# Performance work log

Hardware: AMD Instinct MI355X
Metric: run time of the kernel (lower is better)

## Reference

```python
import jax, jax.numpy as jnp
import numpy as np

N_NODES = 100000
N_EDGES = 3200000
FEAT = 16


def gcn_conv(x, src, dst, W, b):
    # PyG GCNConv: add self-loops, symmetric normalization deg^{-1/2}(A+I)deg^{-1/2},
    # then linear transform and scatter-add aggregation.
    n = x.shape[0]
    loop = jnp.arange(n, dtype=src.dtype)
    s = jnp.concatenate([src, loop])
    d = jnp.concatenate([dst, loop])
    deg = jax.ops.segment_sum(jnp.ones_like(d, dtype=x.dtype), d, num_segments=n)
    dinv = jnp.where(deg > 0, jax.lax.rsqrt(deg), 0.0)
    norm = dinv[s] * dinv[d]  # [E+N]
    h = x @ W  # [N, out]
    msg = h[s] * norm[:, None]  # gather + weight
    out = jax.ops.segment_sum(msg, d, num_segments=n)  # scatter-add
    return out + b


def setup_inputs() -> dict:
    key = jax.random.key(0)
    k1, k2, k3, k4 = jax.random.split(key, 4)
    scale = 1.0 / np.sqrt(FEAT)
    return {
        "x": jax.random.normal(k1, (N_NODES, FEAT), dtype=jnp.float32),
        "edge_index": jax.random.randint(k2, (2, N_EDGES), 0, N_NODES, dtype=jnp.int64) if jax.config.jax_enable_x64 else jax.random.randint(k2, (2, N_EDGES), 0, N_NODES, dtype=jnp.int32),
        "W1": jax.random.normal(k3, (FEAT, 16), dtype=jnp.float32) * scale,
        "b1": jnp.zeros((16,), dtype=jnp.float32),
        "W2": jax.random.normal(k4, (16, FEAT), dtype=jnp.float32) * scale,
        "b2": jnp.zeros((FEAT,), dtype=jnp.float32),
    }


def reference(x, edge_index, W1, b1, W2, b2):
    src, dst = edge_index[0], edge_index[1]
    h = gcn_conv(x, src, dst, W1, b1)
    h = jax.nn.relu(h)
    out = gcn_conv(h, src, dst, W2, b2)
    return out
```

## Files before the change

### kernel.cpp

```cpp
#include <hip/hip_runtime.h>

#define F 16
#define BSHIFT 8
#define NPB 256
#define NB 391
#define CH 4096
#define BCAP 9216


__global__ void init_cursor_kernel(unsigned* __restrict__ cursor) {
    int i = threadIdx.x;
    if (i < NB) cursor[i * 16] = (unsigned)(i * BCAP);
}

__global__ __launch_bounds__(512) void
reorder_kernel(const int* __restrict__ src, const int* __restrict__ dst,
               unsigned* __restrict__ cursor, unsigned* __restrict__ recs, int E) {
    __shared__ unsigned lsorted[CH];
    __shared__ unsigned short lbkt[CH];
    __shared__ unsigned cnt[NB];
    __shared__ unsigned lstart[NB + 1];
    int t = threadIdx.x, b = blockIdx.x;
    int e0 = b * CH;
    int cnt_e = E - e0; if (cnt_e > CH) cnt_e = CH;

    for (int i = t; i < NB; i += 512) cnt[i] = 0;
    __syncthreads();
    unsigned pk[8], rs[8];
#pragma unroll
    for (int j = 0; j < 8; ++j) {
        int i = t + j * 512;
        pk[j] = 0xFFFFFFFFu;
        if (i < cnt_e) {
            unsigned d = (unsigned)dst[e0 + i];
            rs[j] = (unsigned)src[e0 + i];
            unsigned bk = d >> BSHIFT;
            unsigned r = atomicAdd(&cnt[bk], 1u);
            pk[j] = bk | ((d & 255u) << 9) | (r << 17);
        }
    }
    __syncthreads();
    if (t < 64) {
        unsigned run = 0;
        for (int c = 0; c < NB; c += 64) {
            int idx = c + t;
            unsigned v = (idx < NB) ? cnt[idx] : 0u;
            unsigned inc = v;
#pragma unroll
            for (int d = 1; d < 64; d <<= 1) {
                unsigned o = __shfl_up(inc, d, 64);
                if (t >= d) inc += o;
            }
            if (idx < NB) lstart[idx] = run + inc - v;
            run += __shfl(inc, 63, 64);
        }
        if (t == 0) lstart[NB] = (unsigned)cnt_e;
    }
    __syncthreads();
    {
        int s0 = (int)(((unsigned)b * 101u) % (unsigned)NB);
        for (int q = t; q < NB; q += 512) {
            int i = s0 + q; if (i >= NB) i -= NB;
            unsigned c = cnt[i];
            if (c) cnt[i] = atomicAdd(&cursor[i * 16], c);
        }
    }
    __syncthreads();
#pragma unroll
    for (int j = 0; j < 8; ++j) {
        int i = t + j * 512;
        if (i < cnt_e) {
            unsigned p = pk[j];
            unsigned bk = p & 0x1FFu;
            unsigned pos = lstart[bk] + (p >> 17);
            lsorted[pos] = rs[j] | (((p >> 9) & 255u) << 17);
            lbkt[pos] = (unsigned short)bk;
        }
    }
    __syncthreads();
    for (int i = t; i < cnt_e; i += 512) {
        unsigned bk = lbkt[i];
        recs[cnt[bk] + ((unsigned)i - lstart[bk])] = lsorted[i];
    }
}

__global__ __launch_bounds__(1024) void
sort2_kernel(const unsigned* __restrict__ recs, const unsigned* __restrict__ cursor,
             unsigned* __restrict__ srcs, int* __restrict__ noff, int* __restrict__ nend,
             float* __restrict__ dinv, const float* __restrict__ x,
             float* __restrict__ z, int n) {
    __shared__ unsigned lsort[BCAP];
    __shared__ unsigned cnt[NPB];
    __shared__ unsigned ex[NPB];
    __shared__ float ldv[NPB];
    __shared__ unsigned wtot[4];
    int t = threadIdx.x, b = blockIdx.x;
    int e0 = b * BCAP;
    int used = (int)(cursor[b * 16] - (unsigned)e0);
    if (t < NPB) cnt[t] = 0;
    __syncthreads();
    unsigned pk[9], rsr[9];
#pragma unroll
    for (int j = 0; j < 9; ++j) {
        int i = t + j * 1024;
        pk[j] = 0xFFFFFFFFu;
        if (i < used) {
            unsigned rec = recs[e0 + i];
            unsigned node = rec >> 17;
            rsr[j] = rec;
            unsigned r = atomicAdd(&cnt[node], 1u);
            pk[j] = node | (r << 8);
        }
    }
    __syncthreads();
    if (t < NPB) {
        unsigned c = cnt[t];
        unsigned inc = c;
        int lane = t & 63, w = t >> 6;
#pragma unroll
        for (int d = 1; d < 64; d <<= 1) {
            unsigned o = __shfl_up(inc, d, 64);
            if (lane >= d) inc += o;
        }
        if (lane == 63) wtot[w] = inc;
        __syncthreads();
        unsigned wbase = 0;
        for (int i = 0; i < w; ++i) wbase += wtot[i];
        unsigned e = wbase + inc - c;
        ex[t] = e;
        float dv = rsqrtf((float)c + 1.0f);
        ldv[t] = dv;
        int node = b * NPB + t;
        if (node < n) {
            noff[node] = e0 + (int)e;
            nend[node] = e0 + (int)(e + c);
            dinv[node] = dv;
        }
    } else {
        __syncthreads();
    }
    __syncthreads();
#pragma unroll
    for (int j = 0; j < 9; ++j) {
        int i = t + j * 1024;
        if (i < used) {
            unsigned p = pk[j];
            lsort[ex[p & 255u] + (p >> 8)] = rsr[j];
        }
    }
    __syncthreads();
    for (int i = t; i < used; i += 1024) srcs[e0 + i] = lsort[i];
    {
        int node = b * NPB + (t >> 2);
        if (node < n) {
            float4 v = ((const float4*)x)[(size_t)b * 1024 + t];
            float dv = ldv[t >> 2];
            v.x *= dv; v.y *= dv; v.z *= dv; v.w *= dv;
            ((float4*)z)[(size_t)b * 1024 + t] = v;
        }
    }
}

__global__ __launch_bounds__(256) void
agg_bal_kernel(const float* __restrict__ hin, const unsigned* __restrict__ srcs,
               const int* __restrict__ noff, const int* __restrict__ nend,
               const float* __restrict__ dinv,
               const float* __restrict__ W, const float* __restrict__ bias,
               float* __restrict__ outp, int n, int mode) {
    __shared__ float acc[64][F + 1];
    __shared__ float Ws[F * F];
    int t = threadIdx.x, b = blockIdx.x;
    int g = t >> 2, c = t & 3;
    Ws[t] = W[t];
    for (int i = t; i < 64 * (F + 1); i += 256) ((float*)acc)[i] = 0.f;
    __syncthreads();
    int nfirst = b * 64;
    int nlast = nfirst + 63; if (nlast > n - 1) nlast = n - 1;
    int e_start = noff[nfirst];
    int e_end = nend[nlast];
    int T = e_end - e_start;
    int chunk = (T + 63) >> 6;
    int gs = e_start + g * chunk;
    int ge = gs + chunk; if (ge > e_end) ge = e_end;
    const float4* h4 = (const float4*)hin;

#define PROC(r, v)                                                        \
    {                                                                     \
        int nd = (int)((r >> 17) & 63u);                                  \
        if (nd != cur) {                                                  \
            float* a = &acc[cur][c * 4];                                  \
            atomicAdd(a + 0, s.x); atomicAdd(a + 1, s.y);                 \
            atomicAdd(a + 2, s.z); atomicAdd(a + 3, s.w);                 \
            s.x = 0.f; s.y = 0.f; s.z = 0.f; s.w = 0.f;                   \
            cur = nd;                                                     \
        }                                                                 \
        s.x += v.x; s.y += v.y; s.z += v.z; s.w += v.w;                   \
    }

    if (gs < ge) {
        int cur = (int)((srcs[gs] >> 17) & 63u);
        float4 s = {0.f, 0.f, 0.f, 0.f};
        int e = gs;
        for (; e + 4 <= ge; e += 4) {
            unsigned r0 = srcs[e], r1 = srcs[e + 1], r2 = srcs[e + 2], r3 = srcs[e + 3];
            float4 v0 = h4[(size_t)(r0 & 0x1FFFFu) * 4 + c];
            float4 v1 = h4[(size_t)(r1 & 0x1FFFFu) * 4 + c];
            float4 v2 = h4[(size_t)(r2 & 0x1FFFFu) * 4 + c];
            float4 v3 = h4[(size_t)(r3 & 0x1FFFFu) * 4 + c];
            PROC(r0, v0); PROC(r1, v1); PROC(r2, v2); PROC(r3, v3);
        }
        for (; e < ge; ++e) {
            unsigned r0 = srcs[e];
            float4 v0 = h4[(size_t)(r0 & 0x1FFFFu) * 4 + c];
            PROC(r0, v0);
        }
        float* a = &acc[cur][c * 4];
        atomicAdd(a + 0, s.x); atomicAdd(a + 1, s.y);
        atomicAdd(a + 2, s.z); atomicAdd(a + 3, s.w);
    }
#undef PROC
    __syncthreads();
    int node = nfirst + g;
    if (node < n) {
        float4 self = h4[(size_t)node * 4 + c];
        float* ar = &acc[g][c * 4];
        ar[0] += self.x; ar[1] += self.y; ar[2] += self.z; ar[3] += self.w;
    }
    __syncthreads();
    if (node < n) {
        float di = dinv[node];
        float4 o = {0.f, 0.f, 0.f, 0.f};
        int j = c * 4;
#pragma unroll
        for (int k = 0; k < F; ++k) {
            float ak = acc[g][k];
            o.x += ak * Ws[k * F + j + 0];
            o.y += ak * Ws[k * F + j + 1];
            o.z += ak * Ws[k * F + j + 2];
            o.w += ak * Ws[k * F + j + 3];
        }
        float4 bi = ((const float4*)bias)[c];
        o.x = di * o.x + bi.x; o.y = di * o.y + bi.y;
        o.z = di * o.z + bi.z; o.w = di * o.w + bi.w;
        if (mode == 1) {
            o.x = fmaxf(o.x, 0.f) * di; o.y = fmaxf(o.y, 0.f) * di;
            o.z = fmaxf(o.z, 0.f) * di; o.w = fmaxf(o.w, 0.f) * di;
        }
        ((float4*)outp)[(size_t)node * 4 + c] = o;
    }
}


__global__ void deg_kernel(const int* __restrict__ dst, float* __restrict__ deg, int E) {
    int e = blockIdx.x * blockDim.x + threadIdx.x;
    if (e < E) atomicAdd(&deg[dst[e]], 1.0f);
}
__global__ void dinv_kernel(float* __restrict__ deg, int n) {
    int i = blockIdx.x * blockDim.x + threadIdx.x;
    if (i < n) deg[i] = rsqrtf(deg[i] + 1.0f);
}
__global__ void linear2_kernel(const float* __restrict__ in, const float* __restrict__ acc,
                               const float* __restrict__ dinv, const float* __restrict__ W,
                               const float* __restrict__ bias, float* __restrict__ out,
                               int n, int mode) {
    __shared__ float Ws[F * F];
    __shared__ float As[16][F + 1];
    int t = threadIdx.x;
    Ws[t] = W[t];
    int nb = t >> 4, j = t & 15;
    int i = blockIdx.x * 16 + nb;
    float di = 0.f, v = 0.f;
    if (i < n) {
        di = dinv[i]; v = in[i * F + j];
        if (mode) { v = di * (acc[i * F + j] + v) + bias[j]; v = fmaxf(v, 0.f); }
    }
    As[nb][j] = v;
    __syncthreads();
    if (i < n) {
        float s = 0.f;
#pragma unroll
        for (int k = 0; k < F; ++k) s += As[nb][k] * Ws[k * F + j];
        out[i * F + j] = s * di;
    }
}
__global__ void scatter_kernel(const int* __restrict__ src, const int* __restrict__ dst,
                               const float* __restrict__ h, float* __restrict__ acc, int E) {
    int t = blockIdx.x * blockDim.x + threadIdx.x;
    int e = t >> 4, j = t & 15;
    if (e < E) atomicAdd(&acc[dst[e] * F + j], h[src[e] * F + j]);
}
__global__ void out_kernel(const float* __restrict__ acc, const float* __restrict__ h,
                           const float* __restrict__ dinv, const float* __restrict__ bias,
                           float* __restrict__ out, int n) {
    int t = blockIdx.x * blockDim.x + threadIdx.x;
    if (t < n * F) {
        int i = t >> 4, j = t & 15;
        out[t] = dinv[i] * (acc[t] + h[t]) + bias[j];
    }
}


extern "C" void kernel_launch(void* const* d_in, const int* in_sizes, int n_in,
                              void* d_out, int out_size, void* d_ws, size_t ws_size,
                              hipStream_t stream) {
    const float* x  = (const float*)d_in[0];
    const int*   ei = (const int*)d_in[1];
    const float* W1 = (const float*)d_in[2];
    const float* b1 = (const float*)d_in[3];
    const float* W2 = (const float*)d_in[4];
    const float* b2 = (const float*)d_in[5];
    float* outp = (float*)d_out;

    const int N = in_sizes[0] / F;
    const int E = in_sizes[1] / 2;
    const int* src = ei;
    const int* dst = ei + E;

    const int nb_rt = (N + NPB - 1) >> BSHIFT;
    const size_t RC = (size_t)NB * BCAP;
    size_t need = sizeof(unsigned) * ((size_t)N * 19 + 2 * RC + 16 * NB);

    if (nb_rt == NB && E <= CH * 65535 && ws_size >= need) {
        float* dinv = (float*)d_ws;
        float* z = dinv + N;
        unsigned* recs = (unsigned*)(z + (size_t)F * N);
        float* y = (float*)recs;
        unsigned* srcs = recs + RC;
        int* noff = (int*)(srcs + RC);
        int* nend = noff + N;
        unsigned* cursor = (unsigned*)(nend + N);

        init_cursor_kernel<<<1, 512, 0, stream>>>(cursor);
        reorder_kernel<<<(E + CH - 1) / CH, 512, 0, stream>>>(src, dst, cursor, recs, E);
        sort2_kernel<<<NB, 1024, 0, stream>>>(recs, cursor, srcs, noff, nend, dinv, x, z, N);
        agg_bal_kernel<<<(N + 63) / 64, 256, 0, stream>>>(z, srcs, noff, nend, dinv, W1, b1, y, N, 1);
        agg_bal_kernel<<<(N + 63) / 64, 256, 0, stream>>>(y, srcs, noff, nend, dinv, W2, b2, outp, N, 2);
    } else {
        float* dinv = (float*)d_ws;
        float* h = dinv + N;
        float* acc = h + (size_t)F * N;
        hipMemsetAsync(dinv, 0, (size_t)N * sizeof(float), stream);
        hipMemsetAsync(acc, 0, (size_t)F * N * sizeof(float), stream);
        deg_kernel<<<(E + 255) / 256, 256, 0, stream>>>(dst, dinv, E);
        dinv_kernel<<<(N + 255) / 256, 256, 0, stream>>>(dinv, N);
        linear2_kernel<<<(N + 15) / 16, 256, 0, stream>>>(x, nullptr, dinv, W1, nullptr, h, N, 0);
        scatter_kernel<<<((size_t)E * F + 255) / 256, 256, 0, stream>>>(src, dst, h, acc, E);
        linear2_kernel<<<(N + 15) / 16, 256, 0, stream>>>(h, acc, dinv, W2, b1, h, N, 1);
        hipMemsetAsync(acc, 0, (size_t)F * N * sizeof(float), stream);
        scatter_kernel<<<((size_t)E * F + 255) / 256, 256, 0, stream>>>(src, dst, h, acc, E);
        out_kernel<<<((size_t)N * F + 255) / 256, 256, 0, stream>>>(acc, h, dinv, b2, outp, N);
    }
}
```

Baseline: 210.1 us.

## Fuse per-node sort into aggregation kernel, splitting each bucket into four quarter-blocks

```diff
diff --git a/kernel.cpp b/kernel.cpp
--- a/kernel.cpp
+++ b/kernel.cpp
@@ -6,6 +6,7 @@
 #define NB 391
 #define CH 4096
 #define BCAP 9216
+#define QCAP 2432
 
 
 __global__ void init_cursor_kernel(unsigned* __restrict__ cursor) {
@@ -85,104 +86,94 @@
 }
 
 __global__ __launch_bounds__(1024) void
-sort2_kernel(const unsigned* __restrict__ recs, const unsigned* __restrict__ cursor,
-             unsigned* __restrict__ srcs, int* __restrict__ noff, int* __restrict__ nend,
-             float* __restrict__ dinv, const float* __restrict__ x,
-             float* __restrict__ z, int n) {
-    __shared__ unsigned lsort[BCAP];
+histz_kernel(const unsigned* __restrict__ recs, const unsigned* __restrict__ cursor,
+             const float* __restrict__ x, float* __restrict__ z, int n) {
     __shared__ unsigned cnt[NPB];
-    __shared__ unsigned ex[NPB];
     __shared__ float ldv[NPB];
-    __shared__ unsigned wtot[4];
     int t = threadIdx.x, b = blockIdx.x;
     int e0 = b * BCAP;
     int used = (int)(cursor[b * 16] - (unsigned)e0);
     if (t < NPB) cnt[t] = 0;
     __syncthreads();
-    unsigned pk[9], rsr[9];
-#pragma unroll
-    for (int j = 0; j < 9; ++j) {
-        int i = t + j * 1024;
-        pk[j] = 0xFFFFFFFFu;
-        if (i < used) {
-            unsigned rec = recs[e0 + i];
-            unsigned node = rec >> 17;
-            rsr[j] = rec;
-            unsigned r = atomicAdd(&cnt[node], 1u);
-            pk[j] = node | (r << 8);
-        }
-    }
-    __syncthreads();
-    if (t < NPB) {
-        unsigned c = cnt[t];
-        unsigned inc = c;
-        int lane = t & 63, w = t >> 6;
+    for (int i = t; i < used; i += 1024)
+        atomicAdd(&cnt[recs[e0 + i] >> 17], 1u);
+    __syncthreads();
+    if (t < NPB) ldv[t] = rsqrtf((float)cnt[t] + 1.0f);
+    __syncthreads();
+    int node = b * NPB + (t >> 2);
+    if (node < n) {
+        float4 v = ((const float4*)x)[(size_t)b * 1024 + t];
+        float dv = ldv[t >> 2];
+        v.x *= dv; v.y *= dv; v.z *= dv; v.w *= dv;
+        ((float4*)z)[(size_t)b * 1024 + t] = v;
+    }
+}
+
+__global__ __launch_bounds__(256) void
+agg_fused_kernel(const float* __restrict__ hin, const unsigned* __restrict__ recs,
+                 const unsigned* __restrict__ cursor,
+                 const float* __restrict__ W, const float* __restrict__ bias,
+                 float* __restrict__ outp, int n, int mode) {
+    __shared__ unsigned lraw[QCAP];
+    __shared__ unsigned lsort[QCAP];
+    __shared__ float acc[64][F + 1];
+    __shared__ float Ws[F * F];
+    __shared__ unsigned cnt[64];
+    __shared__ unsigned ex[64];
+    __shared__ float ldv[64];
+    __shared__ unsigned nloc_s;
+    int t = threadIdx.x, b = blockIdx.x;
+    int bucket = b >> 2, q = b & 3;
+    int e0 = bucket * BCAP;
+    int used = (int)(cursor[bucket * 16] - (unsigned)e0);
+    int lane = t & 63;
+    Ws[t] = W[t];
+    if (t < 64) cnt[t] = 0;
+    if (t == 0) nloc_s = 0;
+    for (int i = t; i < 64 * (F + 1); i += 256) ((float*)acc)[i] = 0.f;
+    __syncthreads();
+    for (int i = t; i < used; i += 256) {
+        unsigned rec = recs[e0 + i];
+        unsigned node = rec >> 17;
+        bool mine = ((node >> 6) == (unsigned)q);
+        unsigned long long m = __ballot(mine);
+        if (m) {
+            int ldr = __ffsll((long long)m) - 1;
+            unsigned base = 0;
+            if (lane == ldr) base = atomicAdd(&nloc_s, (unsigned)__popcll(m));
+            base = __shfl(base, ldr, 64);
+            if (mine) {
+                unsigned pre = (unsigned)__popcll(m & ((1ull << lane) - 1ull));
+                lraw[base + pre] = rec;
+                atomicAdd(&cnt[node & 63u], 1u);
+            }
+        }
+    }
+    __syncthreads();
+    int nloc = (int)nloc_s;
+    if (t < 64) {
+        unsigned c0 = cnt[t];
+        unsigned inc = c0;
 #pragma unroll
         for (int d = 1; d < 64; d <<= 1) {
             unsigned o = __shfl_up(inc, d, 64);
-            if (lane >= d) inc += o;
-        }
-        if (lane == 63) wtot[w] = inc;
-        __syncthreads();
-        unsigned wbase = 0;
-        for (int i = 0; i < w; ++i) wbase += wtot[i];
-        unsigned e = wbase + inc - c;
-        ex[t] = e;
-        float dv = rsqrtf((float)c + 1.0f);
-        ldv[t] = dv;
-        int node = b * NPB + t;
-        if (node < n) {
-            noff[node] = e0 + (int)e;
-            nend[node] = e0 + (int)(e + c);
-            dinv[node] = dv;
-        }
-    } else {
-        __syncthreads();
-    }
-    __syncthreads();
-#pragma unroll
-    for (int j = 0; j < 9; ++j) {
-        int i = t + j * 1024;
-        if (i < used) {
-            unsigned p = pk[j];
-            lsort[ex[p & 255u] + (p >> 8)] = rsr[j];
-        }
-    }
-    __syncthreads();
-    for (int i = t; i < used; i += 1024) srcs[e0 + i] = lsort[i];
-    {
-        int node = b * NPB + (t >> 2);
-        if (node < n) {
-            float4 v = ((const float4*)x)[(size_t)b * 1024 + t];
-            float dv = ldv[t >> 2];
-            v.x *= dv; v.y *= dv; v.z *= dv; v.w *= dv;
-            ((float4*)z)[(size_t)b * 1024 + t] = v;
-        }
-    }
-}
-
-__global__ __launch_bounds__(256) void
-agg_bal_kernel(const float* __restrict__ hin, const unsigned* __restrict__ srcs,
-               const int* __restrict__ noff, const int* __restrict__ nend,
-               const float* __restrict__ dinv,
-               const float* __restrict__ W, const float* __restrict__ bias,
-               float* __restrict__ outp, int n, int mode) {
-    __shared__ float acc[64][F + 1];
-    __shared__ float Ws[F * F];
-    int t = threadIdx.x, b = blockIdx.x;
+            if (t >= d) inc += o;
+        }
+        ex[t] = inc - c0;
+        ldv[t] = rsqrtf((float)c0 + 1.0f);
+    }
+    __syncthreads();
+    for (int i = t; i < nloc; i += 256) {
+        unsigned rec = lraw[i];
+        unsigned pos = atomicAdd(&ex[(rec >> 17) & 63u], 1u);
+        lsort[pos] = rec;
+    }
+    __syncthreads();
     int g = t >> 2, c = t & 3;
-    Ws[t] = W[t];
-    for (int i = t; i < 64 * (F + 1); i += 256) ((float*)acc)[i] = 0.f;
-    __syncthreads();
-    int nfirst = b * 64;
-    int nlast = nfirst + 63; if (nlast > n - 1) nlast = n - 1;
-    int e_start = noff[nfirst];
-    int e_end = nend[nlast];
-    int T = e_end - e_start;
-    int chunk = (T + 63) >> 6;
-    int gs = e_start + g * chunk;
-    int ge = gs + chunk; if (ge > e_end) ge = e_end;
     const float4* h4 = (const float4*)hin;
+    int chunk = (nloc + 63) >> 6;
+    int gs = g * chunk;
+    int ge = gs + chunk; if (ge > nloc) ge = nloc;
 
 #define PROC(r, v)                                                        \
     {                                                                     \
@@ -198,19 +189,27 @@
     }
 
     if (gs < ge) {
-        int cur = (int)((srcs[gs] >> 17) & 63u);
+        int cur = (int)((lsort[gs] >> 17) & 63u);
         float4 s = {0.f, 0.f, 0.f, 0.f};
         int e = gs;
-        for (; e + 4 <= ge; e += 4) {
-            unsigned r0 = srcs[e], r1 = srcs[e + 1], r2 = srcs[e + 2], r3 = srcs[e + 3];
+        for (; e + 8 <= ge; e += 8) {
+            unsigned r0 = lsort[e + 0], r1 = lsort[e + 1];
+            unsigned r2 = lsort[e + 2], r3 = lsort[e + 3];
+            unsigned r4 = lsort[e + 4], r5 = lsort[e + 5];
+            unsigned r6 = lsort[e + 6], r7 = lsort[e + 7];
             float4 v0 = h4[(size_t)(r0 & 0x1FFFFu) * 4 + c];
             float4 v1 = h4[(size_t)(r1 & 0x1FFFFu) * 4 + c];
             float4 v2 = h4[(size_t)(r2 & 0x1FFFFu) * 4 + c];
             float4 v3 = h4[(size_t)(r3 & 0x1FFFFu) * 4 + c];
+            float4 v4 = h4[(size_t)(r4 & 0x1FFFFu) * 4 + c];
+            float4 v5 = h4[(size_t)(r5 & 0x1FFFFu) * 4 + c];
+            float4 v6 = h4[(size_t)(r6 & 0x1FFFFu) * 4 + c];
+            float4 v7 = h4[(size_t)(r7 & 0x1FFFFu) * 4 + c];
             PROC(r0, v0); PROC(r1, v1); PROC(r2, v2); PROC(r3, v3);
+            PROC(r4, v4); PROC(r5, v5); PROC(r6, v6); PROC(r7, v7);
         }
         for (; e < ge; ++e) {
-            unsigned r0 = srcs[e];
+            unsigned r0 = lsort[e];
             float4 v0 = h4[(size_t)(r0 & 0x1FFFFu) * 4 + c];
             PROC(r0, v0);
         }
@@ -220,7 +219,7 @@
     }
 #undef PROC
     __syncthreads();
-    int node = nfirst + g;
+    int node = bucket * NPB + q * 64 + g;
     if (node < n) {
         float4 self = h4[(size_t)node * 4 + c];
         float* ar = &acc[g][c * 4];
@@ -228,7 +227,7 @@
     }
     __syncthreads();
     if (node < n) {
-        float di = dinv[node];
+        float di = ldv[g];
         float4 o = {0.f, 0.f, 0.f, 0.f};
         int j = c * 4;
 #pragma unroll
@@ -318,23 +317,19 @@
 
     const int nb_rt = (N + NPB - 1) >> BSHIFT;
     const size_t RC = (size_t)NB * BCAP;
-    size_t need = sizeof(unsigned) * ((size_t)N * 19 + 2 * RC + 16 * NB);
+    size_t need = sizeof(unsigned) * ((size_t)N * 32 + RC + 16 * NB);
 
     if (nb_rt == NB && E <= CH * 65535 && ws_size >= need) {
-        float* dinv = (float*)d_ws;
-        float* z = dinv + N;
-        unsigned* recs = (unsigned*)(z + (size_t)F * N);
-        float* y = (float*)recs;
-        unsigned* srcs = recs + RC;
-        int* noff = (int*)(srcs + RC);
-        int* nend = noff + N;
-        unsigned* cursor = (unsigned*)(nend + N);
+        float* z = (float*)d_ws;
+        float* y = z + (size_t)F * N;
+        unsigned* recs = (unsigned*)(y + (size_t)F * N);
+        unsigned* cursor = recs + RC;
 
         init_cursor_kernel<<<1, 512, 0, stream>>>(cursor);
         reorder_kernel<<<(E + CH - 1) / CH, 512, 0, stream>>>(src, dst, cursor, recs, E);
-        sort2_kernel<<<NB, 1024, 0, stream>>>(recs, cursor, srcs, noff, nend, dinv, x, z, N);
-        agg_bal_kernel<<<(N + 63) / 64, 256, 0, stream>>>(z, srcs, noff, nend, dinv, W1, b1, y, N, 1);
-        agg_bal_kernel<<<(N + 63) / 64, 256, 0, stream>>>(y, srcs, noff, nend, dinv, W2, b2, outp, N, 2);
+        histz_kernel<<<NB, 1024, 0, stream>>>(recs, cursor, x, z, N);
+        agg_fused_kernel<<<NB * 4, 256, 0, stream>>>(z, recs, cursor, W1, b1, y, N, 1);
+        agg_fused_kernel<<<NB * 4, 256, 0, stream>>>(y, recs, cursor, W2, b2, outp, N, 2);
     } else {
         float* dinv = (float*)d_ws;
         float* h = dinv + N;
```

Result: slower. 235.1 us (+11.9%).

## Split each node bucket's edges by source half to localize gather reads

Applied to the files above, without the earlier changes.

```diff
diff --git a/kernel.cpp b/kernel.cpp
--- a/kernel.cpp
+++ b/kernel.cpp
@@ -86,18 +86,21 @@
 
 __global__ __launch_bounds__(1024) void
 sort2_kernel(const unsigned* __restrict__ recs, const unsigned* __restrict__ cursor,
-             unsigned* __restrict__ srcs, int* __restrict__ noff, int* __restrict__ nend,
+             unsigned* __restrict__ srcs,
+             int* __restrict__ noffA, int* __restrict__ nendA,
+             int* __restrict__ noffB, int* __restrict__ nendB,
              float* __restrict__ dinv, const float* __restrict__ x,
              float* __restrict__ z, int n) {
     __shared__ unsigned lsort[BCAP];
-    __shared__ unsigned cnt[NPB];
-    __shared__ unsigned ex[NPB];
+    __shared__ unsigned cnt[2 * NPB];
+    __shared__ unsigned ex[2 * NPB];
     __shared__ float ldv[NPB];
-    __shared__ unsigned wtot[4];
+    __shared__ unsigned wtot[8];
     int t = threadIdx.x, b = blockIdx.x;
     int e0 = b * BCAP;
     int used = (int)(cursor[b * 16] - (unsigned)e0);
-    if (t < NPB) cnt[t] = 0;
+    unsigned NH = ((unsigned)n + 1u) >> 1;
+    if (t < 2 * NPB) cnt[t] = 0;
     __syncthreads();
     unsigned pk[9], rsr[9];
 #pragma unroll
@@ -107,37 +110,48 @@
         if (i < used) {
             unsigned rec = recs[e0 + i];
             unsigned node = rec >> 17;
+            unsigned half = ((rec & 0x1FFFFu) >= NH) ? 1u : 0u;
+            unsigned bin = (half << 8) | node;
             rsr[j] = rec;
-            unsigned r = atomicAdd(&cnt[node], 1u);
-            pk[j] = node | (r << 8);
-        }
-    }
-    __syncthreads();
+            unsigned r = atomicAdd(&cnt[bin], 1u);
+            pk[j] = bin | (r << 9);
+        }
+    }
+    __syncthreads();
+    {
+        unsigned c = 0, inc = 0;
+        int lane = t & 63, w = t >> 6;
+        if (t < 2 * NPB) {
+            c = cnt[t];
+            inc = c;
+#pragma unroll
+            for (int d = 1; d < 64; d <<= 1) {
+                unsigned o = __shfl_up(inc, d, 64);
+                if (lane >= d) inc += o;
+            }
+            if (lane == 63) wtot[w] = inc;
+        }
+        __syncthreads();
+        if (t < 2 * NPB) {
+            unsigned wbase = 0;
+            for (int i = 0; i < w; ++i) wbase += wtot[i];
+            unsigned e = wbase + inc - c;
+            ex[t] = e;
+            int node = t & 255, half = t >> 8;
+            int gnode = b * NPB + node;
+            if (gnode < n) {
+                if (half == 0) { noffA[gnode] = e0 + (int)e; nendA[gnode] = e0 + (int)(e + c); }
+                else           { noffB[gnode] = e0 + (int)e; nendB[gnode] = e0 + (int)(e + c); }
+            }
+        }
+        __syncthreads();
+    }
     if (t < NPB) {
-        unsigned c = cnt[t];
-        unsigned inc = c;
-        int lane = t & 63, w = t >> 6;
-#pragma unroll
-        for (int d = 1; d < 64; d <<= 1) {
-            unsigned o = __shfl_up(inc, d, 64);
-            if (lane >= d) inc += o;
-        }
-        if (lane == 63) wtot[w] = inc;
-        __syncthreads();
-        unsigned wbase = 0;
-        for (int i = 0; i < w; ++i) wbase += wtot[i];
-        unsigned e = wbase + inc - c;
-        ex[t] = e;
-        float dv = rsqrtf((float)c + 1.0f);
+        unsigned ctot = cnt[t] + cnt[NPB + t];
+        float dv = rsqrtf((float)ctot + 1.0f);
         ldv[t] = dv;
-        int node = b * NPB + t;
-        if (node < n) {
-            noff[node] = e0 + (int)e;
-            nend[node] = e0 + (int)(e + c);
-            dinv[node] = dv;
-        }
-    } else {
-        __syncthreads();
+        int gnode = b * NPB + t;
+        if (gnode < n) dinv[gnode] = dv;
     }
     __syncthreads();
 #pragma unroll
@@ -145,7 +159,7 @@
         int i = t + j * 1024;
         if (i < used) {
             unsigned p = pk[j];
-            lsort[ex[p & 255u] + (p >> 8)] = rsr[j];
+            lsort[ex[p & 511u] + (p >> 9)] = rsr[j];
         }
     }
     __syncthreads();
@@ -163,7 +177,8 @@
 
 __global__ __launch_bounds__(256) void
 agg_bal_kernel(const float* __restrict__ hin, const unsigned* __restrict__ srcs,
-               const int* __restrict__ noff, const int* __restrict__ nend,
+               const int* __restrict__ noffA, const int* __restrict__ nendA,
+               const int* __restrict__ noffB, const int* __restrict__ nendB,
                const float* __restrict__ dinv,
                const float* __restrict__ W, const float* __restrict__ bias,
                float* __restrict__ outp, int n, int mode) {
@@ -176,12 +191,8 @@
     __syncthreads();
     int nfirst = b * 64;
     int nlast = nfirst + 63; if (nlast > n - 1) nlast = n - 1;
-    int e_start = noff[nfirst];
-    int e_end = nend[nlast];
-    int T = e_end - e_start;
-    int chunk = (T + 63) >> 6;
-    int gs = e_start + g * chunk;
-    int ge = gs + chunk; if (ge > e_end) ge = e_end;
+    int rs0 = noffA[nfirst], re0 = nendA[nlast];
+    int rs1 = noffB[nfirst], re1 = nendB[nlast];
     const float4* h4 = (const float4*)hin;
 
 #define PROC(r, v)                                                        \
@@ -197,29 +208,38 @@
         s.x += v.x; s.y += v.y; s.z += v.z; s.w += v.w;                   \
     }
 
-    if (gs < ge) {
-        int cur = (int)((srcs[gs] >> 17) & 63u);
-        float4 s = {0.f, 0.f, 0.f, 0.f};
-        int e = gs;
-        for (; e + 4 <= ge; e += 4) {
-            unsigned r0 = srcs[e], r1 = srcs[e + 1], r2 = srcs[e + 2], r3 = srcs[e + 3];
-            float4 v0 = h4[(size_t)(r0 & 0x1FFFFu) * 4 + c];
-            float4 v1 = h4[(size_t)(r1 & 0x1FFFFu) * 4 + c];
-            float4 v2 = h4[(size_t)(r2 & 0x1FFFFu) * 4 + c];
-            float4 v3 = h4[(size_t)(r3 & 0x1FFFFu) * 4 + c];
-            PROC(r0, v0); PROC(r1, v1); PROC(r2, v2); PROC(r3, v3);
-        }
-        for (; e < ge; ++e) {
-            unsigned r0 = srcs[e];
-            float4 v0 = h4[(size_t)(r0 & 0x1FFFFu) * 4 + c];
-            PROC(r0, v0);
-        }
-        float* a = &acc[cur][c * 4];
-        atomicAdd(a + 0, s.x); atomicAdd(a + 1, s.y);
-        atomicAdd(a + 2, s.z); atomicAdd(a + 3, s.w);
+#pragma unroll 1
+    for (int p = 0; p < 2; ++p) {
+        int S = p ? rs1 : rs0;
+        int Eend = p ? re1 : re0;
+        int T = Eend - S;
+        int chunk = (T + 63) >> 6;
+        int gs = S + g * chunk;
+        int ge = gs + chunk; if (ge > Eend) ge = Eend;
+        if (gs < ge) {
+            int cur = (int)((srcs[gs] >> 17) & 63u);
+            float4 s = {0.f, 0.f, 0.f, 0.f};
+            int e = gs;
+            for (; e + 4 <= ge; e += 4) {
+                unsigned r0 = srcs[e], r1 = srcs[e + 1], r2 = srcs[e + 2], r3 = srcs[e + 3];
+                float4 v0 = h4[(size_t)(r0 & 0x1FFFFu) * 4 + c];
+                float4 v1 = h4[(size_t)(r1 & 0x1FFFFu) * 4 + c];
+                float4 v2 = h4[(size_t)(r2 & 0x1FFFFu) * 4 + c];
+                float4 v3 = h4[(size_t)(r3 & 0x1FFFFu) * 4 + c];
+                PROC(r0, v0); PROC(r1, v1); PROC(r2, v2); PROC(r3, v3);
+            }
+            for (; e < ge; ++e) {
+                unsigned r0 = srcs[e];
+                float4 v0 = h4[(size_t)(r0 & 0x1FFFFu) * 4 + c];
+                PROC(r0, v0);
+            }
+            float* a = &acc[cur][c * 4];
+            atomicAdd(a + 0, s.x); atomicAdd(a + 1, s.y);
+            atomicAdd(a + 2, s.z); atomicAdd(a + 3, s.w);
+        }
+        __syncthreads();
     }
 #undef PROC
-    __syncthreads();
     int node = nfirst + g;
     if (node < n) {
         float4 self = h4[(size_t)node * 4 + c];
@@ -318,7 +338,7 @@
 
     const int nb_rt = (N + NPB - 1) >> BSHIFT;
     const size_t RC = (size_t)NB * BCAP;
-    size_t need = sizeof(unsigned) * ((size_t)N * 19 + 2 * RC + 16 * NB);
+    size_t need = sizeof(unsigned) * ((size_t)N * 21 + 2 * RC + 16 * NB);
 
     if (nb_rt == NB && E <= CH * 65535 && ws_size >= need) {
         float* dinv = (float*)d_ws;
@@ -326,15 +346,17 @@
         unsigned* recs = (unsigned*)(z + (size_t)F * N);
         float* y = (float*)recs;
         unsigned* srcs = recs + RC;
-        int* noff = (int*)(srcs + RC);
-        int* nend = noff + N;
-        unsigned* cursor = (unsigned*)(nend + N);
+        int* noffA = (int*)(srcs + RC);
+        int* nendA = noffA + N;
+        int* noffB = nendA + N;
+        int* nendB = noffB + N;
+        unsigned* cursor = (unsigned*)(nendB + N);
 
         init_cursor_kernel<<<1, 512, 0, stream>>>(cursor);
         reorder_kernel<<<(E + CH - 1) / CH, 512, 0, stream>>>(src, dst, cursor, recs, E);
-        sort2_kernel<<<NB, 1024, 0, stream>>>(recs, cursor, srcs, noff, nend, dinv, x, z, N);
-        agg_bal_kernel<<<(N + 63) / 64, 256, 0, stream>>>(z, srcs, noff, nend, dinv, W1, b1, y, N, 1);
-        agg_bal_kernel<<<(N + 63) / 64, 256, 0, stream>>>(y, srcs, noff, nend, dinv, W2, b2, outp, N, 2);
+        sort2_kernel<<<NB, 1024, 0, stream>>>(recs, cursor, srcs, noffA, nendA, noffB, nendB, dinv, x, z, N);
+        agg_bal_kernel<<<(N + 63) / 64, 256, 0, stream>>>(z, srcs, noffA, nendA, noffB, nendB, dinv, W1, b1, y, N, 1);
+        agg_bal_kernel<<<(N + 63) / 64, 256, 0, stream>>>(y, srcs, noffA, nendA, noffB, nendB, dinv, W2, b2, outp, N, 2);
     } else {
         float* dinv = (float*)d_ws;
         float* h = dinv + N;
```

After: 205.1 us. -2.4%, faster.
